# Kernel tuning notes

Measured on AMD Instinct MI355X. Metric: run time of the kernel, lower is better.

Reference implementation:

```python
import jax, jax.numpy as jnp
import numpy as np

IMG_SIZE = 640.0
CONF_THRESH = 0.001
NMS_THRESH = 0.6
TOP_K = 1000  # fixed-shape candidate cap per class


def _pairwise_iou(b):
    # b: [K,4] in x1,y1,x2,y2; replicates the numpy NMS math (1e-28 / 1e-14 eps)
    x1, y1, x2, y2 = b[:, 0], b[:, 1], b[:, 2], b[:, 3]
    areas = (x2 - x1) * (y2 - y1)
    xx1 = jnp.maximum(x1[:, None], x1[None, :])
    yy1 = jnp.maximum(y1[:, None], y1[None, :])
    xx2 = jnp.minimum(x2[:, None], x2[None, :])
    yy2 = jnp.minimum(y2[:, None], y2[None, :])
    w = jnp.maximum(1e-28, xx2 - xx1)
    h = jnp.maximum(1e-28, yy2 - yy1)
    inter = w * h
    return inter / (areas[:, None] + areas[None, :] - inter + 1e-14)


def setup_inputs() -> dict:
    key = jax.random.key(0)
    k1, k2, k3 = jax.random.split(key, 3)
    img_size, strides, KA, C = 640, [8, 16, 32], 3, 80
    anchor = np.array([[10, 13], [16, 30], [33, 23], [30, 61], [62, 45], [59, 119],
                       [116, 90], [156, 198], [373, 326]], np.float32).reshape(3, 3, 2)
    grids, anchs, strs = [], [], []
    for lvl, s in enumerate(strides):
        f = img_size // s
        gy, gx = np.meshgrid(np.arange(f), np.arange(f), indexing='ij')
        gxy = np.stack([gx, gy], -1).reshape(-1, 1, 2).astype(np.float32)
        grids.append(np.broadcast_to(gxy, (f * f, KA, 2)).reshape(-1, 2))
        anchs.append(np.broadcast_to(anchor[lvl][None], (f * f, KA, 2)).reshape(-1, 2).astype(np.float32))
        strs.append(np.full((f * f * KA, 1), s, np.float32))
    grid_xy = jnp.asarray(np.concatenate(grids, 0))      # [N,2]
    anchors_wh = jnp.asarray(np.concatenate(anchs, 0))   # [N,2]
    stride_t = jnp.asarray(np.concatenate(strs, 0))      # [N,1]
    N = grid_xy.shape[0]  # 25200
    return {
        'reg_pred': jax.random.normal(k1, (N, 4), jnp.float32),
        'obj_pred': jax.random.normal(k2, (N, 1), jnp.float32),
        'cls_pred': jax.random.normal(k3, (N, C), jnp.float32),
        'grid_xy': grid_xy,
        'anchors_wh': anchors_wh,
        'stride_t': stride_t,
    }


def reference(reg_pred, obj_pred, cls_pred, grid_xy, anchors_wh, stride_t):
    # ---- box decode (YOLO head) ----
    xy = (jax.nn.sigmoid(reg_pred[:, :2]) + grid_xy) * stride_t       # centers in pixels
    wh = jnp.exp(reg_pred[:, 2:]) * anchors_wh                        # sizes in pixels
    boxes = jnp.concatenate([xy - 0.5 * wh, xy + 0.5 * wh], axis=-1)  # [N,4]
    boxes = jnp.clip(boxes / IMG_SIZE, 0.0, 1.0)
    # ---- scoring: sigmoid(obj) * softmax(cls) ----
    scores_all = jax.nn.sigmoid(obj_pred) * jax.nn.softmax(cls_pred, axis=-1)  # [N,C]
    cls_inds = jnp.argmax(scores_all, axis=-1)          # [N]
    scores = jnp.max(scores_all, axis=-1)               # [N]
    C = cls_pred.shape[-1]
    K = TOP_K
    ar = jnp.arange(K)

    def nms_class(c):
        s_c = jnp.where((cls_inds == c) & (scores >= CONF_THRESH), scores, -1.0)
        vals, idx = jax.lax.top_k(s_c, K)               # sorted desc, fixed shape
        b = boxes[idx]                                  # [K,4]
        valid = vals > 0.0
        iou = _pairwise_iou(b)                          # [K,K]

        def body(i, keep):
            sup = keep[i] & (iou[i] > NMS_THRESH) & (ar > i)
            return keep & ~sup

        keep = jax.lax.fori_loop(0, K, body, valid)
        return b, vals, keep

    boxes_out, scores_out, keep = jax.vmap(nms_class)(jnp.arange(C))  # [C,K,4],[C,K],[C,K]
    return boxes_out, scores_out * keep.astype(scores_out.dtype), keep
```

## Files before the change

kernel.cpp:

```cpp
#include <hip/hip_runtime.h>
#include <cstdint>
#include <cstddef>

#define N_CLS 80
#define TOPK 1000
#define POOL_N 2048
#define MCAP 512
#define BD 1024
#define DTB 128
#define LDSB_STRIDE 10
#define SCAN_CHUNK 13

__global__ __launch_bounds__(DTB) void decode_kernel(
    const float* __restrict__ reg, const float* __restrict__ obj,
    const float* __restrict__ cls, const float* __restrict__ grid,
    const float* __restrict__ anch, const float* __restrict__ strd,
    float* __restrict__ boxes, uint2* __restrict__ scs, int N) {
  const int i = blockIdx.x * DTB + threadIdx.x;
  if (i >= N) return;

  const float4 r = ((const float4*)reg)[i];
  const float2 g = ((const float2*)grid)[i];
  const float2 aw = ((const float2*)anch)[i];
  const float st = strd[i];

  float cx = (1.0f / (1.0f + expf(-r.x)) + g.x) * st;
  float cy = (1.0f / (1.0f + expf(-r.y)) + g.y) * st;
  float w = expf(r.z) * aw.x;
  float h = expf(r.w) * aw.y;
  float b0 = fminf(fmaxf((cx - 0.5f * w) / 640.0f, 0.0f), 1.0f);
  float b1 = fminf(fmaxf((cy - 0.5f * h) / 640.0f, 0.0f), 1.0f);
  float b2 = fminf(fmaxf((cx + 0.5f * w) / 640.0f, 0.0f), 1.0f);
  float b3 = fminf(fmaxf((cy + 0.5f * h) / 640.0f, 0.0f), 1.0f);
  float4 bo; bo.x = b0; bo.y = b1; bo.z = b2; bo.w = b3;
  ((float4*)boxes)[i] = bo;

  const float4* cr = (const float4*)cls + (size_t)i * 20;
  float4 x[20];
#pragma unroll
  for (int q = 0; q < 20; ++q) x[q] = cr[q];

  float4 m4 = x[0];
#pragma unroll
  for (int q = 1; q < 20; ++q) {
    m4.x = fmaxf(m4.x, x[q].x); m4.y = fmaxf(m4.y, x[q].y);
    m4.z = fmaxf(m4.z, x[q].z); m4.w = fmaxf(m4.w, x[q].w);
  }
  float mx = fmaxf(fmaxf(m4.x, m4.y), fmaxf(m4.z, m4.w));

#pragma unroll
  for (int q = 0; q < 20; ++q) {
    x[q].x = expf(x[q].x - mx); x[q].y = expf(x[q].y - mx);
    x[q].z = expf(x[q].z - mx); x[q].w = expf(x[q].w - mx);
  }

  float s = 0.0f;
#pragma unroll
  for (int q = 0; q < 20; ++q) {
    s += x[q].x; s += x[q].y; s += x[q].z; s += x[q].w;
  }

  float sig = 1.0f / (1.0f + expf(-obj[i]));

  float best = -1.0f; int bc = 0;
#pragma unroll
  for (int q = 0; q < 20; ++q) {
    float q0 = sig * (x[q].x / s);
    if (q0 > best) { best = q0; bc = 4 * q + 0; }
    float q1 = sig * (x[q].y / s);
    if (q1 > best) { best = q1; bc = 4 * q + 1; }
    float q2 = sig * (x[q].z / s);
    if (q2 > best) { best = q2; bc = 4 * q + 2; }
    float q3 = sig * (x[q].w / s);
    if (q3 > best) { best = q3; bc = 4 * q + 3; }
  }
  scs[i] = make_uint2(__float_as_uint(best), (unsigned)bc);
}

__device__ __forceinline__ unsigned long long kinit(int w, int m) {
  int lo = w << 6;
  return (m <= lo) ? 0ULL : ((m - lo >= 64) ? ~0ULL : ((1ULL << (m - lo)) - 1ULL));
}

__global__ __launch_bounds__(BD) void nms_kernel(
    const float* __restrict__ boxes, const uint2* __restrict__ scs,
    float* __restrict__ out, int N) {
  const int c = blockIdx.x;
  const int tid = threadIdx.x;

  __shared__ uint2 pool[POOL_N];
  __shared__ int pcnt;
  __shared__ float svals[TOPK];
  __shared__ int sidx[TOPK];
  __shared__ __align__(16) float4 bxyz[TOPK];
  __shared__ __align__(16) unsigned long long ldsB[MCAP * LDSB_STRIDE];
  __shared__ unsigned char kp[TOPK];
  __shared__ __align__(16) unsigned long long kmbuf[2][8];
  __shared__ int wsum[BD / 64 + 1];

  if (tid == 0) pcnt = 0;
  __syncthreads();

  for (int b0 = 0; b0 < N; b0 += SCAN_CHUNK * BD) {
    uint2 buf[SCAN_CHUNK];
#pragma unroll
    for (int k = 0; k < SCAN_CHUNK; ++k) {
      int i = b0 + k * BD + tid;
      buf[k] = (i < N) ? scs[i] : make_uint2(0u, 0xFFFFFFFFu);
    }
#pragma unroll
    for (int k = 0; k < SCAN_CHUNK; ++k) {
      int i = b0 + k * BD + tid;
      uint2 sc = buf[k];
      if ((int)sc.y == c && __uint_as_float(sc.x) >= 0.001f) {
        int p = atomicAdd(&pcnt, 1);
        if (p < POOL_N) pool[p] = make_uint2(sc.x, (unsigned)i);
      }
    }
  }
  __syncthreads();

  const int cnt = min(pcnt, POOL_N);
  const int m = min(cnt, TOPK);

  for (int e = tid; e < cnt; e += BD) {
    uint2 me = pool[e];
    float v = __uint_as_float(me.x);
    int idx = (int)me.y;
    int r = 0;
#pragma unroll 8
    for (int k = 0; k < cnt; ++k) {
      uint2 q = pool[k];
      float vk = __uint_as_float(q.x);
      r += (int)((vk > v) || (vk == v && (int)q.y < idx));
    }
    if (r < TOPK) { svals[r] = v; sidx[r] = idx; }
  }
  __syncthreads();

  const int M = TOPK - m;
  if (M > 0) {
    int i = tid;
    bool f = false;
    if (i < N) {
      uint2 sc = scs[i];
      f = !((int)sc.y == c && __uint_as_float(sc.x) >= 0.001f);
    }
    unsigned long long mk = __ballot(f ? 1 : 0);
    int lane = tid & 63, wv = tid >> 6;
    int pre = __popcll(mk & ((1ULL << lane) - 1ULL));
    if (lane == 0) wsum[wv] = __popcll(mk);
    __syncthreads();
    if (tid == 0) {
      int acc = 0;
      for (int wq = 0; wq < BD / 64; ++wq) { int t2 = wsum[wq]; wsum[wq] = acc; acc += t2; }
    }
    __syncthreads();
    int pos = wsum[wv] + pre;
    if (f && pos < M) sidx[m + pos] = i;
  }
  __syncthreads();

  const float4* bf4 = (const float4*)boxes;
  for (int t = tid; t < TOPK; t += BD) bxyz[t] = bf4[sidx[t]];
  __syncthreads();

  const int W = (m + 63) >> 6;
  const bool fast = (m > 0) && (m <= MCAP);
  int cur = 0;

  if (fast) {
    const int tasks = m * W;
    for (int q = tid; q < tasks; q += BD) {
      int w = q / m;
      int j = q - w * m;
      unsigned long long bits = 0ULL;
      if (w <= (j >> 6)) {
        float4 jb = bxyz[j];
        float aj = (jb.z - jb.x) * (jb.w - jb.y);
        int i0 = w << 6, iend = min(i0 + 64, j);
        for (int i = i0; i < iend; ++i) {
          float4 ib = bxyz[i];
          float ai = (ib.z - ib.x) * (ib.w - ib.y);
          float xx1 = fmaxf(ib.x, jb.x), yy1 = fmaxf(ib.y, jb.y);
          float xx2 = fminf(ib.z, jb.z), yy2 = fminf(ib.w, jb.w);
          float ww = fmaxf(1e-28f, xx2 - xx1), hh = fmaxf(1e-28f, yy2 - yy1);
          float inter = ww * hh;
          float iou = inter / (ai + aj - inter + 1e-14f);
          if (iou > 0.6f) bits |= (1ULL << (i - i0));
        }
      }
      ldsB[(size_t)j * LDSB_STRIDE + w] = bits;
    }
    __syncthreads();

    ulonglong2 ta, tb, tc, td;
    ta = tb = tc = td = make_ulonglong2(0ULL, 0ULL);
    if (tid < m) {
      const ulonglong2* rp = (const ulonglong2*)&ldsB[(size_t)tid * LDSB_STRIDE];
      ta = rp[0]; tb = rp[1]; tc = rp[2]; td = rp[3];
    }
    if (tid < 8) kmbuf[0][tid] = kinit(tid, m);
    __syncthreads();

    for (;;) {
      bool keep = false;
      if (tid < m) {
        unsigned long long sup =
            (ta.x & kmbuf[cur][0]) | (ta.y & kmbuf[cur][1]) |
            (tb.x & kmbuf[cur][2]) | (tb.y & kmbuf[cur][3]) |
            (tc.x & kmbuf[cur][4]) | (tc.y & kmbuf[cur][5]) |
            (td.x & kmbuf[cur][6]) | (td.y & kmbuf[cur][7]);
        keep = (sup == 0ULL);
      }
      bool old = (tid < m) &&
                 ((kmbuf[cur][tid >> 6] >> (tid & 63)) & 1ULL);
      unsigned long long bl = __ballot(keep ? 1 : 0);
      int wv = tid >> 6;
      if ((tid & 63) == 0 && wv < 8) kmbuf[cur ^ 1][wv] = bl;
      int any = __syncthreads_or((int)(keep != old));
      cur ^= 1;
      if (!any) break;
    }
  } else {
    for (int t = tid; t < TOPK; t += BD) kp[t] = (t < m) ? 1 : 0;
    __syncthreads();
    for (int i = 0; i < m; ++i) {
      if (kp[i]) {
        float4 rb = bxyz[i];
        float ai = (rb.z - rb.x) * (rb.w - rb.y);
        for (int j = i + 1 + tid; j < m; j += BD) {
          if (kp[j]) {
            float4 jb = bxyz[j];
            float aj = (jb.z - jb.x) * (jb.w - jb.y);
            float xx1 = fmaxf(rb.x, jb.x), yy1 = fmaxf(rb.y, jb.y);
            float xx2 = fminf(rb.z, jb.z), yy2 = fminf(rb.w, jb.w);
            float ww = fmaxf(1e-28f, xx2 - xx1), hh = fmaxf(1e-28f, yy2 - yy1);
            float inter = ww * hh;
            float iou = inter / (ai + aj - inter + 1e-14f);
            if (iou > 0.6f) kp[j] = 0;
          }
        }
      }
      __syncthreads();
    }
  }

  float* outB = out;
  float* outS = out + N_CLS * TOPK * 4;
  float* outK = outS + N_CLS * TOPK;
  for (int t = tid; t < TOPK; t += BD) {
    float k = 0.0f;
    if (t < m)
      k = fast ? (float)((kmbuf[cur][t >> 6] >> (t & 63)) & 1ULL)
               : (float)kp[t];
    float v = (t < m) ? svals[t] : -1.0f;
    ((float4*)outB)[c * TOPK + t] = bxyz[t];
    outS[c * TOPK + t] = v * k;
    outK[c * TOPK + t] = k;
  }
}

extern "C" void kernel_launch(void* const* d_in, const int* in_sizes, int n_in,
                              void* d_out, int out_size, void* d_ws, size_t ws_size,
                              hipStream_t stream) {
  const float* reg  = (const float*)d_in[0];
  const float* obj  = (const float*)d_in[1];
  const float* cls  = (const float*)d_in[2];
  const float* grid = (const float*)d_in[3];
  const float* anch = (const float*)d_in[4];
  const float* strd = (const float*)d_in[5];
  const int N = in_sizes[0] / 4;

  char* w8 = (char*)d_ws;
  size_t off = 0;
  float* boxes = (float*)(w8 + off); off += (size_t)N * 16;
  uint2* scs   = (uint2*)(w8 + off); off += (size_t)N * 8;
  float* out = (float*)d_out;

  decode_kernel<<<(N + DTB - 1) / DTB, DTB, 0, stream>>>(
      reg, obj, cls, grid, anch, strd, boxes, scs, N);
  nms_kernel<<<N_CLS, BD, 0, stream>>>(boxes, scs, out, N);
}
```

Before: 115.7 us.

## Bucket candidates per class in decode kernel instead of full rescans in NMS

The decode kernel now bins each anchor by its argmax class into per-block, per-class slices using shared-memory atomics, and writes per-block counts. The NMS kernel then gathers only its own class's candidates through a prefix sum over the 25 blocks, rather than each of the 80 blocks scanning all 25200 scores. This removes a large redundant global read per class. In exchange, decode runs as only 25 blocks of 1024 threads, which lowers occupancy for that kernel. Each slice is capped at 128 entries, which could drop candidates if one class is heavily concentrated within a block.

```diff
diff --git a/kernel.cpp b/kernel.cpp
--- a/kernel.cpp
+++ b/kernel.cpp
@@ -7,74 +7,95 @@
 #define POOL_N 2048
 #define MCAP 512
 #define BD 1024
-#define DTB 128
+#define DTB2 1024
+#define NBLK 25
+#define SLICE 128
 #define LDSB_STRIDE 10
-#define SCAN_CHUNK 13
-
-__global__ __launch_bounds__(DTB) void decode_kernel(
+
+__global__ __launch_bounds__(DTB2) void decode_kernel(
     const float* __restrict__ reg, const float* __restrict__ obj,
     const float* __restrict__ cls, const float* __restrict__ grid,
     const float* __restrict__ anch, const float* __restrict__ strd,
-    float* __restrict__ boxes, uint2* __restrict__ scs, int N) {
-  const int i = blockIdx.x * DTB + threadIdx.x;
-  if (i >= N) return;
-
-  const float4 r = ((const float4*)reg)[i];
-  const float2 g = ((const float2*)grid)[i];
-  const float2 aw = ((const float2*)anch)[i];
-  const float st = strd[i];
-
-  float cx = (1.0f / (1.0f + expf(-r.x)) + g.x) * st;
-  float cy = (1.0f / (1.0f + expf(-r.y)) + g.y) * st;
-  float w = expf(r.z) * aw.x;
-  float h = expf(r.w) * aw.y;
-  float b0 = fminf(fmaxf((cx - 0.5f * w) / 640.0f, 0.0f), 1.0f);
-  float b1 = fminf(fmaxf((cy - 0.5f * h) / 640.0f, 0.0f), 1.0f);
-  float b2 = fminf(fmaxf((cx + 0.5f * w) / 640.0f, 0.0f), 1.0f);
-  float b3 = fminf(fmaxf((cy + 0.5f * h) / 640.0f, 0.0f), 1.0f);
-  float4 bo; bo.x = b0; bo.y = b1; bo.z = b2; bo.w = b3;
-  ((float4*)boxes)[i] = bo;
-
-  const float4* cr = (const float4*)cls + (size_t)i * 20;
-  float4 x[20];
-#pragma unroll
-  for (int q = 0; q < 20; ++q) x[q] = cr[q];
-
-  float4 m4 = x[0];
-#pragma unroll
-  for (int q = 1; q < 20; ++q) {
-    m4.x = fmaxf(m4.x, x[q].x); m4.y = fmaxf(m4.y, x[q].y);
-    m4.z = fmaxf(m4.z, x[q].z); m4.w = fmaxf(m4.w, x[q].w);
-  }
-  float mx = fmaxf(fmaxf(m4.x, m4.y), fmaxf(m4.z, m4.w));
-
-#pragma unroll
-  for (int q = 0; q < 20; ++q) {
-    x[q].x = expf(x[q].x - mx); x[q].y = expf(x[q].y - mx);
-    x[q].z = expf(x[q].z - mx); x[q].w = expf(x[q].w - mx);
-  }
-
-  float s = 0.0f;
-#pragma unroll
-  for (int q = 0; q < 20; ++q) {
-    s += x[q].x; s += x[q].y; s += x[q].z; s += x[q].w;
-  }
-
-  float sig = 1.0f / (1.0f + expf(-obj[i]));
-
-  float best = -1.0f; int bc = 0;
-#pragma unroll
-  for (int q = 0; q < 20; ++q) {
-    float q0 = sig * (x[q].x / s);
-    if (q0 > best) { best = q0; bc = 4 * q + 0; }
-    float q1 = sig * (x[q].y / s);
-    if (q1 > best) { best = q1; bc = 4 * q + 1; }
-    float q2 = sig * (x[q].z / s);
-    if (q2 > best) { best = q2; bc = 4 * q + 2; }
-    float q3 = sig * (x[q].w / s);
-    if (q3 > best) { best = q3; bc = 4 * q + 3; }
-  }
-  scs[i] = make_uint2(__float_as_uint(best), (unsigned)bc);
+    float* __restrict__ boxes, uint2* __restrict__ scs,
+    int* __restrict__ cnts, uint2* __restrict__ gpool2, int N) {
+  __shared__ int hcnt[N_CLS];
+  const int blk = blockIdx.x;
+  const int tid = threadIdx.x;
+  const int i = blk * DTB2 + tid;
+
+  if (tid < N_CLS) hcnt[tid] = 0;
+  __syncthreads();
+
+  const bool valid = (i < N);
+  float best = -1.0f;
+  int bc = 0;
+
+  if (valid) {
+    const float4 r = ((const float4*)reg)[i];
+    const float2 g = ((const float2*)grid)[i];
+    const float2 aw = ((const float2*)anch)[i];
+    const float st = strd[i];
+
+    float cx = (1.0f / (1.0f + expf(-r.x)) + g.x) * st;
+    float cy = (1.0f / (1.0f + expf(-r.y)) + g.y) * st;
+    float w = expf(r.z) * aw.x;
+    float h = expf(r.w) * aw.y;
+    float b0 = fminf(fmaxf((cx - 0.5f * w) / 640.0f, 0.0f), 1.0f);
+    float b1 = fminf(fmaxf((cy - 0.5f * h) / 640.0f, 0.0f), 1.0f);
+    float b2 = fminf(fmaxf((cx + 0.5f * w) / 640.0f, 0.0f), 1.0f);
+    float b3 = fminf(fmaxf((cy + 0.5f * h) / 640.0f, 0.0f), 1.0f);
+    float4 bo; bo.x = b0; bo.y = b1; bo.z = b2; bo.w = b3;
+    ((float4*)boxes)[i] = bo;
+
+    const float4* cr = (const float4*)cls + (size_t)i * 20;
+    float4 x[20];
+#pragma unroll
+    for (int q = 0; q < 20; ++q) x[q] = cr[q];
+
+    float4 m4 = x[0];
+#pragma unroll
+    for (int q = 1; q < 20; ++q) {
+      m4.x = fmaxf(m4.x, x[q].x); m4.y = fmaxf(m4.y, x[q].y);
+      m4.z = fmaxf(m4.z, x[q].z); m4.w = fmaxf(m4.w, x[q].w);
+    }
+    float mx = fmaxf(fmaxf(m4.x, m4.y), fmaxf(m4.z, m4.w));
+
+#pragma unroll
+    for (int q = 0; q < 20; ++q) {
+      x[q].x = expf(x[q].x - mx); x[q].y = expf(x[q].y - mx);
+      x[q].z = expf(x[q].z - mx); x[q].w = expf(x[q].w - mx);
+    }
+
+    float s = 0.0f;
+#pragma unroll
+    for (int q = 0; q < 20; ++q) {
+      s += x[q].x; s += x[q].y; s += x[q].z; s += x[q].w;
+    }
+
+    float sig = 1.0f / (1.0f + expf(-obj[i]));
+
+#pragma unroll
+    for (int q = 0; q < 20; ++q) {
+      float q0 = sig * (x[q].x / s);
+      if (q0 > best) { best = q0; bc = 4 * q + 0; }
+      float q1 = sig * (x[q].y / s);
+      if (q1 > best) { best = q1; bc = 4 * q + 1; }
+      float q2 = sig * (x[q].z / s);
+      if (q2 > best) { best = q2; bc = 4 * q + 2; }
+      float q3 = sig * (x[q].w / s);
+      if (q3 > best) { best = q3; bc = 4 * q + 3; }
+    }
+    scs[i] = make_uint2(__float_as_uint(best), (unsigned)bc);
+  }
+
+  const bool pos = valid && (best >= 0.001f);
+  int slot = -1;
+  if (pos) slot = atomicAdd(&hcnt[bc], 1);
+  __syncthreads();
+  if (tid < N_CLS) cnts[tid * NBLK + blk] = min(hcnt[tid], SLICE);
+  if (pos && slot < SLICE)
+    gpool2[((size_t)bc * NBLK + blk) * SLICE + slot] =
+        make_uint2(__float_as_uint(best), (unsigned)i);
 }
 
 __device__ __forceinline__ unsigned long long kinit(int w, int m) {
@@ -84,12 +105,12 @@
 
 __global__ __launch_bounds__(BD) void nms_kernel(
     const float* __restrict__ boxes, const uint2* __restrict__ scs,
+    const int* __restrict__ cnts, const uint2* __restrict__ gpool2,
     float* __restrict__ out, int N) {
   const int c = blockIdx.x;
   const int tid = threadIdx.x;
 
   __shared__ uint2 pool[POOL_N];
-  __shared__ int pcnt;
   __shared__ float svals[TOPK];
   __shared__ int sidx[TOPK];
   __shared__ __align__(16) float4 bxyz[TOPK];
@@ -97,31 +118,30 @@
   __shared__ unsigned char kp[TOPK];
   __shared__ __align__(16) unsigned long long kmbuf[2][8];
   __shared__ int wsum[BD / 64 + 1];
-
-  if (tid == 0) pcnt = 0;
-  __syncthreads();
-
-  for (int b0 = 0; b0 < N; b0 += SCAN_CHUNK * BD) {
-    uint2 buf[SCAN_CHUNK];
-#pragma unroll
-    for (int k = 0; k < SCAN_CHUNK; ++k) {
-      int i = b0 + k * BD + tid;
-      buf[k] = (i < N) ? scs[i] : make_uint2(0u, 0xFFFFFFFFu);
-    }
-#pragma unroll
-    for (int k = 0; k < SCAN_CHUNK; ++k) {
-      int i = b0 + k * BD + tid;
-      uint2 sc = buf[k];
-      if ((int)sc.y == c && __uint_as_float(sc.x) >= 0.001f) {
-        int p = atomicAdd(&pcnt, 1);
-        if (p < POOL_N) pool[p] = make_uint2(sc.x, (unsigned)i);
-      }
-    }
-  }
-  __syncthreads();
-
-  const int cnt = min(pcnt, POOL_N);
+  __shared__ int pref[NBLK + 1];
+
+  if (tid == 0) {
+    int acc = 0;
+    pref[0] = 0;
+    const int* cc = cnts + c * NBLK;
+#pragma unroll
+    for (int b = 0; b < NBLK; ++b) {
+      acc = min(acc + cc[b], POOL_N);
+      pref[b + 1] = acc;
+    }
+  }
+  __syncthreads();
+  const int cnt = pref[NBLK];
   const int m = min(cnt, TOPK);
+
+  const uint2* gp = gpool2 + (size_t)c * NBLK * SLICE;
+  for (int t = tid; t < cnt; t += BD) {
+    int b = 0;
+#pragma unroll
+    for (int q = 0; q < NBLK; ++q) b += (int)(t >= pref[q + 1]);
+    pool[t] = gp[(size_t)b * SLICE + (t - pref[b])];
+  }
+  __syncthreads();
 
   for (int e = tid; e < cnt; e += BD) {
     uint2 me = pool[e];
@@ -274,11 +294,13 @@
 
   char* w8 = (char*)d_ws;
   size_t off = 0;
-  float* boxes = (float*)(w8 + off); off += (size_t)N * 16;
-  uint2* scs   = (uint2*)(w8 + off); off += (size_t)N * 8;
+  float* boxes  = (float*)(w8 + off); off += (size_t)N * 16;
+  uint2* scs    = (uint2*)(w8 + off); off += (size_t)N * 8;
+  int*   cnts   = (int*)(w8 + off);   off += (size_t)N_CLS * NBLK * 4;
+  uint2* gpool2 = (uint2*)(w8 + off); off += (size_t)N_CLS * NBLK * SLICE * 8;
   float* out = (float*)d_out;
 
-  decode_kernel<<<(N + DTB - 1) / DTB, DTB, 0, stream>>>(
-      reg, obj, cls, grid, anch, strd, boxes, scs, N);
-  nms_kernel<<<N_CLS, BD, 0, stream>>>(boxes, scs, out, N);
+  decode_kernel<<<NBLK, DTB2, 0, stream>>>(
+      reg, obj, cls, grid, anch, strd, boxes, scs, cnts, gpool2, N);
+  nms_kernel<<<N_CLS, BD, 0, stream>>>(boxes, scs, cnts, gpool2, out, N);
 }
```

Result: slower. 124.6 us (+7.7%).
